# Optimization experiments

Hardware: AMD Instinct MI355X
Metric: run time of the kernel (lower is better)

Reference implementation:

```python
import jax, jax.numpy as jnp
import numpy as np

B, T, I, H, O = 128, 4096, 6, 32, 2


def setup_inputs() -> dict:
    key = jax.random.key(0)
    ks = jax.random.split(key, 8)
    x = jax.random.normal(ks[0], (B, T, I), dtype=jnp.float32)
    lengths = jax.random.randint(ks[1], (B,), 1, T + 1, dtype=jnp.int32)
    lengths = jnp.sort(lengths)[::-1]            # descending (enforce_sorted=True)
    lengths = lengths.at[0].set(T)               # max length == T -> static output shape
    s = 1.0 / np.sqrt(H)                         # PyTorch GRU/Linear init scale
    w_ih = jax.random.uniform(ks[2], (3 * H, I), minval=-s, maxval=s, dtype=jnp.float32)
    w_hh = jax.random.uniform(ks[3], (3 * H, H), minval=-s, maxval=s, dtype=jnp.float32)
    b_ih = jax.random.uniform(ks[4], (3 * H,), minval=-s, maxval=s, dtype=jnp.float32)
    b_hh = jax.random.uniform(ks[5], (3 * H,), minval=-s, maxval=s, dtype=jnp.float32)
    fc_w = jax.random.uniform(ks[6], (O, H), minval=-s, maxval=s, dtype=jnp.float32)
    fc_b = jax.random.uniform(ks[7], (O,), minval=-s, maxval=s, dtype=jnp.float32)
    return {"x": x, "lengths": lengths, "w_ih": w_ih, "w_hh": w_hh,
            "b_ih": b_ih, "b_hh": b_hh, "fc_w": fc_w, "fc_b": fc_b}


def reference(x, lengths, w_ih, w_hh, b_ih, b_hh, fc_w, fc_b):
    Bn, Tn, _ = x.shape
    Hn = w_hh.shape[1]
    # Precompute input-side gate projections for all steps (one big GEMM).
    gx = jnp.einsum('bti,gi->btg', x, w_ih) + b_ih      # [B,T,3H] (gate order: r,z,n)
    gx = jnp.swapaxes(gx, 0, 1)                          # [T,B,3H] time-major for scan
    mask = jnp.arange(Tn)[:, None] < lengths[None, :]    # [T,B] valid-step mask
    h0 = jnp.zeros((Bn, Hn), x.dtype)

    def step(h, inp):
        gxt, m = inp                                     # gxt [B,3H], m [B]
        gh = h @ w_hh.T + b_hh                           # [B,3H]
        xr, xz, xn = jnp.split(gxt, 3, axis=-1)
        hr, hz, hn = jnp.split(gh, 3, axis=-1)
        r = jax.nn.sigmoid(xr + hr)
        z = jax.nn.sigmoid(xz + hz)
        n = jnp.tanh(xn + r * hn)
        h_new = (1.0 - z) * n + z * h
        m = m[:, None]
        out = jnp.where(m, h_new, 0.0)                   # pad_packed pads with zeros
        h = jnp.where(m, h_new, h)                       # freeze state past length
        return h, out

    _, ys = jax.lax.scan(step, h0, (gx, mask))           # ys [T,B,H]
    out = jnp.swapaxes(ys, 0, 1)                         # [B,T,H]
    # fc applied to every (incl. zero-padded) timestep, as in the torch code
    return jnp.einsum('bth,oh->bto', out, fc_w) + fc_b   # [B,T,O]
```

## Files before the change

### kernel.cpp

```cpp
#include <hip/hip_runtime.h>

#define TT 4096
#define BB 128
#define L2E 1.4426950408889634f

typedef unsigned uv2 __attribute__((ext_vector_type(2)));
typedef float v2f __attribute__((ext_vector_type(2)));
typedef float v4f __attribute__((ext_vector_type(4)));
typedef __bf16 v8bf __attribute__((ext_vector_type(8)));

__device__ __forceinline__ float fexp2(float a) { return __builtin_amdgcn_exp2f(a); }

__device__ __forceinline__ float bpermf(int idx_bytes, float v) {
  return __int_as_float(__builtin_amdgcn_ds_bpermute(idx_bytes, __float_as_int(v)));
}

__device__ __forceinline__ float xhalf_sum(float p) {
#if __has_builtin(__builtin_amdgcn_permlane32_swap)
  uv2 r = __builtin_amdgcn_permlane32_swap(__float_as_uint(p), __float_as_uint(p),
                                           false, false);
  return __uint_as_float(r[0]) + __uint_as_float(r[1]);
#else
  return p + bpermf((threadIdx.x ^ 32) << 2, p);
#endif
}

__device__ __forceinline__ unsigned cvtpk(float lo, float hi) {
  unsigned r;
  asm("v_cvt_pk_bf16_f32 %0, %1, %2" : "=v"(r) : "v"(lo), "v"(hi));
  return r;
}

template <int CTRL>
__device__ __forceinline__ int dppmv(int src) {
  return __builtin_amdgcn_update_dpp(0, src, CTRL, 0xF, 0xF, true);
}

__device__ __forceinline__ v8bf frag_from(unsigned u0, unsigned u1, unsigned u2,
                                          unsigned u3) {
  uint4 uu = make_uint4(u0, u1, u2, u3);
  return __builtin_bit_cast(v8bf, uu);
}

__global__ __launch_bounds__(256) void gx_pre(
    const float* __restrict__ x, const float* __restrict__ w_ih,
    const float* __restrict__ b_ih, const float* __restrict__ b_hh,
    const int* __restrict__ lengths, float* __restrict__ gx) {
  const size_t idx = (size_t)blockIdx.x * 256 + threadIdx.x;
  const int g = (int)(idx % 96);
  const size_t bt = idx / 96;
  const int b = (int)(bt >> 12);
  const int t = (int)(bt & (TT - 1));
  if (t >= lengths[b]) return;
  const float* xp = x + bt * 6;
  float acc = (g < 64) ? (b_ih[g] + b_hh[g]) : b_ih[g];
#pragma unroll
  for (int i = 0; i < 6; ++i) acc = fmaf(w_ih[g * 6 + i], xp[i], acc);
  gx[idx] = (g < 64) ? (L2E * acc) : (2.0f * L2E * acc);
}

__global__ __launch_bounds__(64) __attribute__((amdgpu_waves_per_eu(1, 1)))
void gru_seq(const int* __restrict__ lengths, const float* __restrict__ w_hh,
             const float* __restrict__ b_hh, const float* __restrict__ gx,
             float* __restrict__ hbuf) {
  __shared__ alignas(16) float hring[2][32][32];

  const int b = blockIdx.x;
  const int l = threadIdx.x;
  const int j = l & 31;
  const int len = lengths[b];
  const int n_ = l & 15;
  const int g = l >> 4;
  const int koff = 16 * (g & 1) + 8 * (g >> 1);

  const int q_ = (l >> 2) & 3;
  const int qb = 2 * (l >> 5);
  const int s0 = (q_ - qb) & 3;
  const int s1 = (q_ - qb - 1) & 3;
  const bool s0a = s0 & 1, s0b = s0 & 2;
  const bool s1a = s1 & 1, s1b = s1 & 2;

  auto make_wfrag = [&](int grow, int jb, float scale) -> v8bf {
    const float* wrow = w_hh + (grow + jb + n_) * 32 + koff;
    unsigned u0 = cvtpk(wrow[0] * scale, wrow[1] * scale);
    unsigned u1 = cvtpk(wrow[2] * scale, wrow[3] * scale);
    unsigned u2 = cvtpk(wrow[4] * scale, wrow[5] * scale);
    unsigned u3 = cvtpk(wrow[6] * scale, wrow[7] * scale);
    return frag_from(u0, u1, u2, u3);
  };
  const v8bf fR0 = make_wfrag(0, 0, L2E),          fR1 = make_wfrag(0, 16, L2E);
  const v8bf fZ0 = make_wfrag(32, 0, L2E),         fZ1 = make_wfrag(32, 16, L2E);
  const v8bf fN0 = make_wfrag(64, 0, 2.0f * L2E),  fN1 = make_wfrag(64, 16, 2.0f * L2E);
  v4f cn0, cn1;
  {
    const float c0 = 2.0f * L2E * b_hh[64 + n_];
    const float c1 = 2.0f * L2E * b_hh[80 + n_];
    cn0 = v4f{c0, c0, c0, c0};
    cn1 = v4f{c1, c1, c1, c1};
  }
  const v4f zero4 = v4f{0.f, 0.f, 0.f, 0.f};
  const bool hiSel = (g & 1);

  const float* gxb = gx + (size_t)b * TT * 96;
  float* hrow = hbuf + (size_t)b * TT * 32;

  float h = 0.0f;
  int t = 0;

  float g0r, g0z, g0n, g1r, g1z, g1n, g2r, g2z, g2n, g3r, g3z, g3n;
  float g4r, g4z, g4n, g5r, g5z, g5n, g6r, g6z, g6n, g7r, g7z, g7n;
  {
    auto ld = [&](int ti, float& R, float& Z, float& N) {
      const int tc = (ti < len) ? ti : (len - 1);
      const float* p = gxb + (size_t)tc * 96;
      R = p[j]; Z = p[32 + j]; N = p[64 + j];
    };
    ld(0, g0r, g0z, g0n); ld(1, g1r, g1z, g1n);
    ld(2, g2r, g2z, g2n); ld(3, g3r, g3z, g3n);
    ld(4, g4r, g4z, g4n); ld(5, g5r, g5z, g5n);
    ld(6, g6r, g6z, g6n); ld(7, g7r, g7z, g7n);
  }

  auto flush = [&](int base, int cnt) {
    const float4* src = (const float4*)(&hring[(base >> 5) & 1][0][0]);
    float4* dst = (float4*)(hrow + (size_t)base * 32);
    const int n4 = cnt * 8;
    for (int qq = l; qq < n4; qq += 64) dst[qq] = src[qq];
  };

  auto step = [&](float& GR, float& GZ, float& GN) {
    const float xr_ = GR, xz_ = GZ, xn_ = GN;
    {
      const int tp = (t + 8 < len) ? (t + 8) : (len - 1);
      const float* gp = gxb + (size_t)tp * 96;
      GR = gp[j]; GZ = gp[32 + j]; GN = gp[64 + j];
    }

    const int hi_ = __float_as_int(h);
    const int qa = dppmv<0x00>(hi_), qbv = dppmv<0x55>(hi_);
    const int qc = dppmv<0xAA>(hi_), qd = dppmv<0xFF>(hi_);
    const unsigned u0 = cvtpk(__int_as_float(qa), __int_as_float(qbv));
    const unsigned u1 = cvtpk(__int_as_float(qc), __int_as_float(qd));
    const int r4u0 = dppmv<0x124>((int)u0), r8u0 = dppmv<0x128>((int)u0),
              r12u0 = dppmv<0x12C>((int)u0);
    const int r4u1 = dppmv<0x124>((int)u1), r8u1 = dppmv<0x128>((int)u1),
              r12u1 = dppmv<0x12C>((int)u1);
    const unsigned d0 = s0b ? (s0a ? (unsigned)r12u0 : (unsigned)r8u0)
                            : (s0a ? (unsigned)r4u0 : u0);
    const unsigned d1 = s0b ? (s0a ? (unsigned)r12u1 : (unsigned)r8u1)
                            : (s0a ? (unsigned)r4u1 : u1);
    const unsigned d2 = s1b ? (s1a ? (unsigned)r12u0 : (unsigned)r8u0)
                            : (s1a ? (unsigned)r4u0 : u0);
    const unsigned d3 = s1b ? (s1a ? (unsigned)r12u1 : (unsigned)r8u1)
                            : (s1a ? (unsigned)r4u1 : u1);
    const v8bf ha = frag_from(d0, d1, d2, d3);

    const v4f yr0 = __builtin_amdgcn_mfma_f32_16x16x32_bf16(ha, fR0, zero4, 0, 0, 0);
    const v4f yr1 = __builtin_amdgcn_mfma_f32_16x16x32_bf16(ha, fR1, zero4, 0, 0, 0);
    const v4f yz0 = __builtin_amdgcn_mfma_f32_16x16x32_bf16(ha, fZ0, zero4, 0, 0, 0);
    const v4f yz1 = __builtin_amdgcn_mfma_f32_16x16x32_bf16(ha, fZ1, zero4, 0, 0, 0);
    const v4f yn0 = __builtin_amdgcn_mfma_f32_16x16x32_bf16(ha, fN0, cn0, 0, 0, 0);
    const v4f yn1 = __builtin_amdgcn_mfma_f32_16x16x32_bf16(ha, fN1, cn1, 0, 0, 0);

    const float yr = hiSel ? yr1[0] : yr0[0];
    const float yz = hiSel ? yz1[0] : yz0[0];
    const float hn = hiSel ? yn1[0] : yn0[0];

    const float r_ = __builtin_amdgcn_rcpf(1.0f + fexp2(-(yr + xr_)));
    const float z_ = __builtin_amdgcn_rcpf(1.0f + fexp2(-(yz + xz_)));
    const float ap = fmaf(r_, hn, xn_);
    const float q0 = __builtin_amdgcn_rcpf(1.0f + fexp2(-ap));
    const float nn = fmaf(2.0f, q0, -1.0f);
    h = fmaf(z_, h - nn, nn);

    hring[(t >> 5) & 1][t & 31][j] = h;
    if ((t & 31) == 31) flush(t - 31, 32);
    ++t;
  };

  while (t + 8 <= len) {
    step(g0r, g0z, g0n);
    step(g1r, g1z, g1n);
    step(g2r, g2z, g2n);
    step(g3r, g3z, g3n);
    step(g4r, g4z, g4n);
    step(g5r, g5z, g5n);
    step(g6r, g6z, g6n);
    step(g7r, g7z, g7n);
  }
  if (t < len) step(g0r, g0z, g0n);
  if (t < len) step(g1r, g1z, g1n);
  if (t < len) step(g2r, g2z, g2n);
  if (t < len) step(g3r, g3z, g3n);
  if (t < len) step(g4r, g4z, g4n);
  if (t < len) step(g5r, g5z, g5n);
  if (t < len) step(g6r, g6z, g6n);

  const int rem = len & 31;
  if (rem) flush(len - rem, rem);
}

__global__ __launch_bounds__(256) void fc_apply(
    const float* __restrict__ hbuf, const int* __restrict__ lengths,
    const float* __restrict__ fc_w, const float* __restrict__ fc_b,
    float* __restrict__ out) {
  const int idx = blockIdx.x * 256 + threadIdx.x;
  const int b = idx >> 12;
  const int t = idx & (TT - 1);
  const float fb0 = fc_b[0], fb1 = fc_b[1];
  float* op = out + (size_t)idx * 2;
  if (t >= lengths[b]) {
    op[0] = fb0;
    op[1] = fb1;
    return;
  }
  const float4* hp = (const float4*)(hbuf + (size_t)idx * 32);
  const float4* w0 = (const float4*)(fc_w);
  const float4* w1 = (const float4*)(fc_w + 32);
  float o0 = 0.f, o1 = 0.f;
#pragma unroll
  for (int qq = 0; qq < 8; ++qq) {
    const float4 hv = hp[qq], a = w0[qq], c = w1[qq];
    o0 += hv.x * a.x + hv.y * a.y + hv.z * a.z + hv.w * a.w;
    o1 += hv.x * c.x + hv.y * c.y + hv.z * c.z + hv.w * c.w;
  }
  op[0] = o0 + fb0;
  op[1] = o1 + fb1;
}

__global__ __launch_bounds__(64) void gru_fallback(
    const float* __restrict__ x, const int* __restrict__ lengths,
    const float* __restrict__ w_ih, const float* __restrict__ w_hh,
    const float* __restrict__ b_ih, const float* __restrict__ b_hh,
    const float* __restrict__ fc_w, const float* __restrict__ fc_b,
    float* __restrict__ out) {
  const int b = blockIdx.x;
  const int l = threadIdx.x;
  const int j = l & 31;
  const int half = l >> 5;
  const int ko = half << 4;
  const int len = lengths[b];

  float wr[16], wz[16], wn[16];
#pragma unroll
  for (int k = 0; k < 16; ++k) wr[k] = w_hh[j * 32 + ko + k] * L2E;
#pragma unroll
  for (int k = 0; k < 16; ++k) wz[k] = w_hh[(32 + j) * 32 + ko + k] * L2E;
#pragma unroll
  for (int k = 0; k < 16; ++k) wn[k] = w_hh[(64 + j) * 32 + ko + k] * (2.0f * L2E);
  float wxr[6], wxz[6], wxn[6];
#pragma unroll
  for (int i = 0; i < 6; ++i) wxr[i] = w_ih[j * 6 + i] * (0.5f * L2E);
#pragma unroll
  for (int i = 0; i < 6; ++i) wxz[i] = w_ih[(32 + j) * 6 + i] * (0.5f * L2E);
#pragma unroll
  for (int i = 0; i < 6; ++i) wxn[i] = w_ih[(64 + j) * 6 + i] * (2.0f * L2E);
  const float br = (b_ih[j] + b_hh[j]) * (0.5f * L2E);
  const float bz = (b_ih[32 + j] + b_hh[32 + j]) * (0.5f * L2E);
  const float bxn = b_ih[64 + j] * (2.0f * L2E);
  const float bhn = b_hh[64 + j] * L2E;
  const float fcw = fc_w[half * 32 + j];
  const float fcb = fc_b[half];

  const float* xb = x + (size_t)b * (TT * 6);
  float* ob = out + (size_t)b * (TT * 2);
  const int bko = half << 6;
  float h = 0.0f;

  v2f cx[3], nx[3];
  {
    const v2f* xp = (const v2f*)xb;
    cx[0] = xp[0]; cx[1] = xp[1]; cx[2] = xp[2];
  }
  for (int t = 0; t < len; ++t) {
    const int tn = (t + 1 < len) ? (t + 1) : t;
    const v2f* xp = (const v2f*)(xb + tn * 6);
    nx[0] = xp[0]; nx[1] = xp[1]; nx[2] = xp[2];
    float xr = br, xz = bz, xn = bxn;
#pragma unroll
    for (int i = 0; i < 3; ++i) {
      const float c0 = cx[i][0], c1 = cx[i][1];
      xr = fmaf(wxr[2 * i], c0, xr); xr = fmaf(wxr[2 * i + 1], c1, xr);
      xz = fmaf(wxz[2 * i], c0, xz); xz = fmaf(wxz[2 * i + 1], c1, xz);
      xn = fmaf(wxn[2 * i], c0, xn); xn = fmaf(wxn[2 * i + 1], c1, xn);
    }
    float hbv[16];
#pragma unroll
    for (int k = 0; k < 16; ++k) hbv[k] = bpermf(bko + (k << 2), h);
    float ar0 = xr, ar1 = 0.f, az0 = xz, az1 = 0.f, an0 = bhn, an1 = 0.f;
#pragma unroll
    for (int k = 0; k < 8; ++k) {
      ar0 = fmaf(wr[k], hbv[k], ar0);
      ar1 = fmaf(wr[k + 8], hbv[k + 8], ar1);
      az0 = fmaf(wz[k], hbv[k], az0);
      az1 = fmaf(wz[k + 8], hbv[k + 8], az1);
      an0 = fmaf(wn[k], hbv[k], an0);
      an1 = fmaf(wn[k + 8], hbv[k + 8], an1);
    }
    const float sr = xhalf_sum(ar0 + ar1);
    const float r = __builtin_amdgcn_rcpf(1.0f + fexp2(-sr));
    const float sz = xhalf_sum(az0 + az1);
    const float z = __builtin_amdgcn_rcpf(1.0f + fexp2(-sz));
    const float hn = xhalf_sum(an0 + an1);
    const float ap = fmaf(r, hn, xn);
    const float qq = __builtin_amdgcn_rcpf(1.0f + fexp2(-ap));
    const float nn = fmaf(2.0f, qq, -1.0f);
    h = fmaf(z, h - nn, nn);
    float p = h * fcw;
    p += __shfl_xor(p, 1);
    p += __shfl_xor(p, 2);
    p += __shfl_xor(p, 4);
    p += __shfl_xor(p, 8);
    p += __shfl_xor(p, 16);
    if (j == 0) ob[t * 2 + half] = p + fcb;
#pragma unroll
    for (int i = 0; i < 3; ++i) cx[i] = nx[i];
  }
  const float fb0 = fc_b[0], fb1 = fc_b[1];
  for (int idx = len * 2 + l; idx < TT * 2; idx += 64)
    ob[idx] = (idx & 1) ? fb1 : fb0;
}

extern "C" void kernel_launch(void* const* d_in, const int* in_sizes, int n_in,
                              void* d_out, int out_size, void* d_ws, size_t ws_size,
                              hipStream_t stream) {
  const float* x       = (const float*)d_in[0];
  const int*   lengths = (const int*)d_in[1];
  const float* w_ih    = (const float*)d_in[2];
  const float* w_hh    = (const float*)d_in[3];
  const float* b_ih    = (const float*)d_in[4];
  const float* b_hh    = (const float*)d_in[5];
  const float* fc_w    = (const float*)d_in[6];
  const float* fc_b    = (const float*)d_in[7];
  float* outp = (float*)d_out;

  const size_t hbuf_elems = (size_t)BB * TT * 32;
  const size_t gx_elems   = (size_t)BB * TT * 96;
  const size_t need = (hbuf_elems + gx_elems) * sizeof(float);
  if (ws_size >= need) {
    float* hbuf = (float*)d_ws;
    float* gx = (float*)d_ws + hbuf_elems;
    hipLaunchKernelGGL(gx_pre, dim3((BB * TT * 96) / 256), dim3(256), 0, stream,
                       x, w_ih, b_ih, b_hh, lengths, gx);
    hipLaunchKernelGGL(gru_seq, dim3(BB), dim3(64), 0, stream,
                       lengths, w_hh, b_hh, gx, hbuf);
    hipLaunchKernelGGL(fc_apply, dim3((BB * TT) / 256), dim3(256), 0, stream,
                       hbuf, lengths, fc_w, fc_b, outp);
  } else {
    hipLaunchKernelGGL(gru_fallback, dim3(BB), dim3(64), 0, stream,
                       x, lengths, w_ih, w_hh, b_ih, b_hh, fc_w, fc_b, outp);
  }
}
```

Baseline: 820.5 us.

## Fuse fc projection into GRU recurrence flush and drop hbuf workspace

The output linear layer is now applied inside the sequential GRU kernel when each 32-step ring of hidden states is flushed. Each lane holds one fc row in registers and computes dot products from LDS, so the full hidden-state buffer is never written to global memory and the separate fc_apply launch is gone. Padded tail outputs are filled with the bias at the end of the kernel. This removes a large global write/read round trip and one launch, but it adds compute and register pressure to the latency-bound serial kernel.

```diff
diff --git a/kernel.cpp b/kernel.cpp
--- a/kernel.cpp
+++ b/kernel.cpp
@@ -62,7 +62,8 @@
 __global__ __launch_bounds__(64) __attribute__((amdgpu_waves_per_eu(1, 1)))
 void gru_seq(const int* __restrict__ lengths, const float* __restrict__ w_hh,
              const float* __restrict__ b_hh, const float* __restrict__ gx,
-             float* __restrict__ hbuf) {
+             const float* __restrict__ fc_w, const float* __restrict__ fc_b,
+             float* __restrict__ out) {
   __shared__ alignas(16) float hring[2][32][32];
 
   const int b = blockIdx.x;
@@ -101,8 +102,18 @@
   const v4f zero4 = v4f{0.f, 0.f, 0.f, 0.f};
   const bool hiSel = (g & 1);
 
+  const int o_ = l >> 5;
+  float4 fcw4[8];
+  {
+    const float4* wp = (const float4*)(fc_w + o_ * 32);
+#pragma unroll
+    for (int qq = 0; qq < 8; ++qq) fcw4[qq] = wp[qq];
+  }
+  const float fcb_ = fc_b[o_];
+  const float fb0 = fc_b[0], fb1 = fc_b[1];
+
   const float* gxb = gx + (size_t)b * TT * 96;
-  float* hrow = hbuf + (size_t)b * TT * 32;
+  float* ob = out + (size_t)b * TT * 2;
 
   float h = 0.0f;
   int t = 0;
@@ -122,10 +133,17 @@
   }
 
   auto flush = [&](int base, int cnt) {
-    const float4* src = (const float4*)(&hring[(base >> 5) & 1][0][0]);
-    float4* dst = (float4*)(hrow + (size_t)base * 32);
-    const int n4 = cnt * 8;
-    for (int qq = l; qq < n4; qq += 64) dst[qq] = src[qq];
+    const int i = l & 31;
+    if (i < cnt) {
+      const float4* hp = (const float4*)(&hring[(base >> 5) & 1][i][0]);
+      float acc = 0.f;
+#pragma unroll
+      for (int qq = 0; qq < 8; ++qq) {
+        const float4 hv = hp[qq], w = fcw4[qq];
+        acc += hv.x * w.x + hv.y * w.y + hv.z * w.z + hv.w * w.w;
+      }
+      ob[(base + i) * 2 + o_] = acc + fcb_;
+    }
   };
 
   auto step = [&](float& GR, float& GZ, float& GN) {
@@ -198,34 +216,9 @@
 
   const int rem = len & 31;
   if (rem) flush(len - rem, rem);
-}
-
-__global__ __launch_bounds__(256) void fc_apply(
-    const float* __restrict__ hbuf, const int* __restrict__ lengths,
-    const float* __restrict__ fc_w, const float* __restrict__ fc_b,
-    float* __restrict__ out) {
-  const int idx = blockIdx.x * 256 + threadIdx.x;
-  const int b = idx >> 12;
-  const int t = idx & (TT - 1);
-  const float fb0 = fc_b[0], fb1 = fc_b[1];
-  float* op = out + (size_t)idx * 2;
-  if (t >= lengths[b]) {
-    op[0] = fb0;
-    op[1] = fb1;
-    return;
-  }
-  const float4* hp = (const float4*)(hbuf + (size_t)idx * 32);
-  const float4* w0 = (const float4*)(fc_w);
-  const float4* w1 = (const float4*)(fc_w + 32);
-  float o0 = 0.f, o1 = 0.f;
-#pragma unroll
-  for (int qq = 0; qq < 8; ++qq) {
-    const float4 hv = hp[qq], a = w0[qq], c = w1[qq];
-    o0 += hv.x * a.x + hv.y * a.y + hv.z * a.z + hv.w * a.w;
-    o1 += hv.x * c.x + hv.y * c.y + hv.z * c.z + hv.w * c.w;
-  }
-  op[0] = o0 + fb0;
-  op[1] = o1 + fb1;
+
+  for (int idx2 = len * 2 + l; idx2 < TT * 2; idx2 += 64)
+    ob[idx2] = (idx2 & 1) ? fb1 : fb0;
 }
 
 __global__ __launch_bounds__(64) void gru_fallback(
@@ -334,18 +327,14 @@
   const float* fc_b    = (const float*)d_in[7];
   float* outp = (float*)d_out;
 
-  const size_t hbuf_elems = (size_t)BB * TT * 32;
-  const size_t gx_elems   = (size_t)BB * TT * 96;
-  const size_t need = (hbuf_elems + gx_elems) * sizeof(float);
+  const size_t gx_elems = (size_t)BB * TT * 96;
+  const size_t need = gx_elems * sizeof(float);
   if (ws_size >= need) {
-    float* hbuf = (float*)d_ws;
-    float* gx = (float*)d_ws + hbuf_elems;
+    float* gx = (float*)d_ws;
     hipLaunchKernelGGL(gx_pre, dim3((BB * TT * 96) / 256), dim3(256), 0, stream,
                        x, w_ih, b_ih, b_hh, lengths, gx);
     hipLaunchKernelGGL(gru_seq, dim3(BB), dim3(64), 0, stream,
-                       lengths, w_hh, b_hh, gx, hbuf);
-    hipLaunchKernelGGL(fc_apply, dim3((BB * TT) / 256), dim3(256), 0, stream,
-                       hbuf, lengths, fc_w, fc_b, outp);
+                       lengths, w_hh, b_hh, gx, fc_w, fc_b, outp);
   } else {
     hipLaunchKernelGGL(gru_fallback, dim3(BB), dim3(64), 0, stream,
                        x, lengths, w_ih, w_hh, b_ih, b_hh, fc_w, fc_b, outp);
```

Measured after the change: 808.0 us. No clear change (-1.5%).
